# Kernel optimization log

Measured on AMD Instinct MI355X. Metric: run time of the kernel, lower is better.

The kernel has to match this reference:

```python
import jax, jax.numpy as jnp
import numpy as np

BN_EPS = 1e-5


def gcn_conv(x, src, dst, W, b):
    # PyG GCNConv: add self-loops, symmetric normalization, bias after aggregation
    n = x.shape[0]
    h = x @ W                                   # [N, d]
    deg = jnp.zeros((n,), x.dtype).at[dst].add(1.0) + 1.0  # in-degree + self-loop
    dinv = jax.lax.rsqrt(deg)
    norm = dinv[src] * dinv[dst]                # [E]
    agg = jnp.zeros_like(h).at[dst].add(h[src] * norm[:, None])
    agg = agg + h * (dinv * dinv)[:, None]      # self-loop messages
    return agg + b


def batchnorm(x, gamma, beta):
    mu = x.mean(0)
    var = x.var(0)  # biased, as torch BN training mode
    return (x - mu) * jax.lax.rsqrt(var + BN_EPS) * gamma + beta


def mha(x, w_in, b_in, w_out, b_out, n_heads=4):
    # torch nn.MultiheadAttention, input [L, N, E]
    L, N, d = x.shape
    hd = d // n_heads
    qkv = x @ w_in.T + b_in                     # [L, N, 3d]
    q, k, v = jnp.split(qkv, 3, axis=-1)
    rh = lambda t: t.reshape(L, N, n_heads, hd)
    q = rh(q) * (1.0 / np.sqrt(hd))
    k, v = rh(k), rh(v)
    scores = jnp.einsum('lnhd,mnhd->nhlm', q, k)
    a = jax.nn.softmax(scores, axis=-1)
    o = jnp.einsum('nhlm,mnhd->lnhd', a, v).reshape(L, N, d)
    return o @ w_out.T + b_out


def setup_inputs() -> dict:
    key = jax.random.key(0)
    N, d, E, L, R = 50000, 128, 400000, 3, 4
    ks = jax.random.split(key, 12)
    s = 1.0 / np.sqrt(d)
    return {
        'features': jax.random.normal(ks[0], (N, d), jnp.float32),
        'rel_emb': jax.random.normal(ks[1], (R, d), jnp.float32),
        'edge_index': jax.random.randint(ks[2], (R, 2, E), 0, N, dtype=jnp.int32),
        'W_gcn': jax.random.normal(ks[3], (L, d, d), jnp.float32) * s,
        'b_gcn': jnp.zeros((L, d), jnp.float32),
        'bn_gamma': jnp.ones((L - 1, d), jnp.float32),
        'bn_beta': jnp.zeros((L - 1, d), jnp.float32),
        'W_rt': jax.random.normal(ks[4], (L, d, d), jnp.float32) * s,
        'b_rt': jnp.zeros((L, d), jnp.float32),
        'attn_w_in': jax.random.normal(ks[5], (3 * d, d), jnp.float32) * s,
        'attn_b_in': jnp.zeros((3 * d,), jnp.float32),
        'attn_w_out': jax.random.normal(ks[6], (d, d), jnp.float32) * s,
        'attn_b_out': jnp.zeros((d,), jnp.float32),
        'alphas': jnp.full((4,), 0.95, jnp.float32),
        'fusion_q': jax.random.normal(ks[7], (d,), jnp.float32),
        'fusion_w': jax.random.normal(ks[8], (d, d), jnp.float32) * s,
        'fusion_b': jnp.zeros((d,), jnp.float32),
    }


def reference(features, rel_emb, edge_index, W_gcn, b_gcn, bn_gamma, bn_beta,
              W_rt, b_rt, attn_w_in, attn_b_in, attn_w_out, attn_b_out,
              alphas, fusion_q, fusion_w, fusion_b):
    L = W_gcn.shape[0]
    # RelationGCN unpacks rel_emb as (poi_r, s_r, d_r, n_r) and processes
    # relations in order (n, poi, s, d) -> permute to processing order.
    perm = jnp.array([3, 0, 1, 2])
    rels = rel_emb[perm]                # [4, d], order (n, poi, s, d)
    edges = edge_index[perm]            # [4, 2, E]
    embs = jnp.broadcast_to(features, (4,) + features.shape)  # all start at features

    def inner(emb, r, src, dst, Wg, bg, gamma, beta):
        h = gcn_conv(emb * r, src, dst, Wg, bg)
        return emb + jax.nn.leaky_relu(batchnorm(h, gamma, beta))

    for i in range(L - 1):
        embs = jax.vmap(inner, in_axes=(0, 0, 0, 0, None, None, None, None))(
            embs, rels, edges[:, 0], edges[:, 1],
            W_gcn[i], b_gcn[i], bn_gamma[i], bn_beta[i])
        rels = rels @ W_rt[i].T + b_rt[i]
        # dropout p=0.0 -> identity

    embs = jax.vmap(lambda e, r, s_, t_: gcn_conv(e * r, s_, t_, W_gcn[-1], b_gcn[-1]))(
        embs, rels, edges[:, 0], edges[:, 1])
    rels = rels @ W_rt[-1].T + b_rt[-1]

    # PM_Model mis-unpacks RelationGCN outputs (returned order n,poi,s,d as
    # poi,s,d,n). CrossLayer then stacks (n_emb, poi_emb, d_emb, s_emb) which in
    # true processing order is (d, n, s, poi):
    stk = jnp.stack([embs[3], embs[0], embs[2], embs[1]])  # [4, N, d]
    fusion = mha(stk, attn_w_in, attn_b_in, attn_w_out, attn_b_out)
    a = alphas  # [alpha_n, alpha_poi, alpha_d, alpha_s]
    n_f = fusion[0] * a[0] + (1 - a[0]) * stk[0]
    poi_f = fusion[1] * a[1] + (1 - a[1]) * stk[1]
    d_f = fusion[2] * a[2] + (1 - a[2]) * stk[2]
    s_f = fusion[3] * a[3] + (1 - a[3]) * stk[3]

    def score(f):
        return jnp.mean(jnp.sum(jax.nn.leaky_relu(f @ fusion_w.T + fusion_b) * fusion_q, axis=1))

    w = jax.nn.softmax(jnp.stack([score(n_f), score(poi_f), score(s_f), score(d_f)]))
    region = w[0] * n_f + w[1] * poi_f + w[2] * s_f + w[3] * d_f

    # Final multiplies use the same mis-unpacked rel names:
    # n_r<-rels[3](true d), poi_r<-rels[0](true n), s_r<-rels[1], d_r<-rels[2]
    return (region, region * rels[3], region * rels[0], region * rels[1], region * rels[2])
```

## Files before the change

kernel.cpp:

```cpp
#include <hip/hip_runtime.h>
#include <cstdio>

#define DD 128
#define NREL 4

using short8 = __attribute__((ext_vector_type(8))) short;
using f32x4  = __attribute__((ext_vector_type(4))) float;

struct PtrB4 { const unsigned short* p[4]; };
struct OutB4 { unsigned short* p[4]; };

__device__ __forceinline__ int edge_perm(int r) { return (r + 3) & 3; }

__device__ __forceinline__ float bf_lo(unsigned u) { return __uint_as_float(u << 16); }
__device__ __forceinline__ float bf_hi(unsigned u) { return __uint_as_float(u & 0xffff0000u); }
__device__ __forceinline__ float bfe(short s) {
  return __uint_as_float(((unsigned)(unsigned short)s) << 16);
}
__device__ __forceinline__ unsigned short f2bf(float f) {
  unsigned x = __float_as_uint(f);
  unsigned r = (x + 0x7fffu + ((x >> 16) & 1u)) >> 16;
  return (unsigned short)r;
}
__device__ __forceinline__ unsigned pack2(float a, float b) {
  return (unsigned)f2bf(a) | ((unsigned)f2bf(b) << 16);
}


__global__ void rels_init(const float* __restrict__ rel_emb, float* __restrict__ rels) {
  int t = threadIdx.x;
  int r = t >> 7, c = t & 127;
  rels[t] = rel_emb[edge_perm(r) * DD + c];
}

__global__ void rels_update(const float* __restrict__ rin, const float* __restrict__ Wrt,
                            const float* __restrict__ brt, float* __restrict__ rout) {
  int t = threadIdx.x;
  int r = t >> 7, j = t & 127;
  float s = brt[j];
  const float* wr = Wrt + j * DD;
  const float* xr = rin + r * DD;
  for (int c = 0; c < DD; ++c) s += xr[c] * wr[c];
  rout[t] = s;
}

__global__ void scale_w_bf(const float* __restrict__ rels_i, const float* __restrict__ Wg,
                           unsigned short* __restrict__ Wsb) {
  int i = blockIdx.x * 256 + threadIdx.x;
  int r = i >> 14, rem = i & 16383, j = rem >> 7, c = rem & 127;
  Wsb[i] = f2bf(rels_i[r * DD + c] * Wg[c * DD + j]);
}

__global__ void conv_w(const float* __restrict__ w_in, const float* __restrict__ w_out,
                       const float* __restrict__ w_fus, unsigned short* __restrict__ Wab) {
  int i = blockIdx.x * 256 + threadIdx.x;
  float v = (i < 49152) ? w_in[i] : (i < 65536 ? w_out[i - 49152] : w_fus[i - 65536]);
  Wab[i] = f2bf(v);
}

__global__ void conv_f2b(const float* __restrict__ in, unsigned* __restrict__ out2, size_t n4) {
  size_t i = (size_t)blockIdx.x * 256 + threadIdx.x;
  if (i < n4) {
    float4 v = ((const float4*)in)[i];
    out2[i * 2]     = pack2(v.x, v.y);
    out2[i * 2 + 1] = pack2(v.z, v.w);
  }
}


__global__ void count_deg(const int* __restrict__ ei, int* __restrict__ deg, int N, int E) {
  int r = blockIdx.y;
  int base = blockIdx.x * 1024 + threadIdx.x;
  const int* dsts = ei + (size_t)edge_perm(r) * 2 * E + E;
#pragma unroll
  for (int k = 0; k < 4; ++k) {
    int e = base + k * 256;
    if (e < E) atomicAdd(deg + (size_t)r * N + dsts[e], 1);
  }
}

__global__ void finalize_dinv(const int* __restrict__ deg, float* __restrict__ dinv, int total) {
  int i = blockIdx.x * 256 + threadIdx.x;
  if (i < total) dinv[i] = rsqrtf((float)deg[i] + 1.0f);
}

__global__ void scan_block(const int* __restrict__ deg, int* __restrict__ excl,
                           int* __restrict__ bsums, int n) {
  __shared__ int sh[256];
  int i = blockIdx.x * 256 + threadIdx.x;
  int v = (i < n) ? deg[i] : 0;
  sh[threadIdx.x] = v;
  __syncthreads();
  for (int st = 1; st < 256; st <<= 1) {
    int t = (threadIdx.x >= st) ? sh[threadIdx.x - st] : 0;
    __syncthreads();
    sh[threadIdx.x] += t;
    __syncthreads();
  }
  if (i < n) excl[i] = sh[threadIdx.x] - v;
  if (threadIdx.x == 255) bsums[blockIdx.x] = sh[255];
}

__global__ void scan_sums(int* __restrict__ bsums, int nb) {
  __shared__ int sh[1024];
  int v = (threadIdx.x < nb) ? bsums[threadIdx.x] : 0;
  sh[threadIdx.x] = v;
  __syncthreads();
  for (int st = 1; st < 1024; st <<= 1) {
    int t = (threadIdx.x >= st) ? sh[threadIdx.x - st] : 0;
    __syncthreads();
    sh[threadIdx.x] += t;
    __syncthreads();
  }
  if (threadIdx.x < nb) bsums[threadIdx.x] = sh[threadIdx.x] - v;
}

__global__ void scan_add(int* __restrict__ excl, int* __restrict__ cursor,
                         const int* __restrict__ bsums, int n) {
  int i = blockIdx.x * 256 + threadIdx.x;
  if (i < n) {
    int o = excl[i] + bsums[blockIdx.x];
    excl[i] = o;
    cursor[i] = o;
  }
}

__global__ void fill_edges(const int* __restrict__ ei, int* __restrict__ cursor,
                           int* __restrict__ srcbuf, int N, int E) {
  int r = blockIdx.y;
  int base = blockIdx.x * 1024 + threadIdx.x;
  const int* bp = ei + (size_t)edge_perm(r) * 2 * E;
  int s[4], d[4], pos[4];
#pragma unroll
  for (int k = 0; k < 4; ++k) {
    int e = base + k * 256;
    s[k] = (e < E) ? bp[e] : 0;
    d[k] = (e < E) ? bp[E + e] : 0;
  }
#pragma unroll
  for (int k = 0; k < 4; ++k) {
    int e = base + k * 256;
    if (e < E) pos[k] = atomicAdd(&cursor[r * N + d[k]], 1);
  }
#pragma unroll
  for (int k = 0; k < 4; ++k) {
    int e = base + k * 256;
    if (e < E) srcbuf[pos[k]] = r * N + s[k];
  }
}

template <int MODE>
__global__ __launch_bounds__(256) void gemm_ws(PtrB4 xs, PtrB4 wz, OutB4 ys,
                                               const float* __restrict__ bias,
                                               const float* __restrict__ dinv,
                                               const float* __restrict__ fq,
                                               float* __restrict__ S,
                                               PtrB4 stks,
                                               const float* __restrict__ alphas,
                                               int M) {
  int z = blockIdx.y;
  const unsigned short* __restrict__ X = xs.p[z];
  const unsigned short* __restrict__ W = wz.p[z];
  int tid = threadIdx.x;
  int wave = tid >> 6, lane = tid & 63;
  int r16 = lane & 15, kgrp = lane >> 4;
  int rowhalf = wave >> 1, colbase = (wave & 1) * 64;
  int blockrow = blockIdx.x * 64;

  short8 b[4][4];
#pragma unroll
  for (int s = 0; s < 4; ++s)
#pragma unroll
    for (int cn = 0; cn < 4; ++cn)
      b[s][cn] = *(const short8*)(W + ((colbase + cn * 16 + r16) << 7) + s * 32 + kgrp * 8);

  int row0 = blockrow + rowhalf * 32 + r16;
  int r0c = row0 < M ? row0 : M - 1;
  int r1c = row0 + 16 < M ? row0 + 16 : M - 1;
  short8 a[2][4];
#pragma unroll
  for (int s = 0; s < 4; ++s) {
    a[0][s] = *(const short8*)(X + (size_t)r0c * DD + s * 32 + kgrp * 8);
    a[1][s] = *(const short8*)(X + (size_t)r1c * DD + s * 32 + kgrp * 8);
  }

  f32x4 acc[2][4];
#pragma unroll
  for (int rt = 0; rt < 2; ++rt)
#pragma unroll
    for (int cn = 0; cn < 4; ++cn)
#pragma unroll
      for (int j = 0; j < 4; ++j) acc[rt][cn][j] = 0.f;

#pragma unroll
  for (int s = 0; s < 4; ++s)
#pragma unroll
    for (int rt = 0; rt < 2; ++rt)
#pragma unroll
      for (int cn = 0; cn < 4; ++cn)
        acc[rt][cn] = __builtin_amdgcn_mfma_f32_16x16x32_bf16(a[rt][s], b[s][cn], acc[rt][cn], 0, 0, 0);

  __shared__ float red[256];
  if constexpr (MODE == 2) {
    float ss = 0.f;
#pragma unroll
    for (int rt = 0; rt < 2; ++rt)
#pragma unroll
      for (int cn = 0; cn < 4; ++cn) {
        int col = colbase + cn * 16 + r16;
        float bb = bias[col];
        float qc = fq[col];
#pragma unroll
        for (int i = 0; i < 4; ++i) {
          int row = blockrow + rowhalf * 32 + rt * 16 + kgrp * 4 + i;
          if (row < M) {
            float y = acc[rt][cn][i] + bb;
            float v = y > 0.f ? y : 0.01f * y;
            ss += v * qc;
          }
        }
      }
    red[tid] = ss;
    __syncthreads();
    for (int st = 128; st > 0; st >>= 1) {
      if (tid < st) red[tid] += red[tid + st];
      __syncthreads();
    }
    if (tid == 0) atomicAdd(S + z, red[0]);
  } else {
    __shared__ __align__(16) unsigned short tile[64][DD + 8];
    float dv[2][4];
    if constexpr (MODE == 0) {
#pragma unroll
      for (int rt = 0; rt < 2; ++rt)
#pragma unroll
        for (int i = 0; i < 4; ++i) {
          int row = blockrow + rowhalf * 32 + rt * 16 + kgrp * 4 + i;
          dv[rt][i] = dinv[(size_t)z * M + (row < M ? row : 0)];
        }
    }
#pragma unroll
    for (int rt = 0; rt < 2; ++rt)
#pragma unroll
      for (int cn = 0; cn < 4; ++cn) {
        int col = colbase + cn * 16 + r16;
        float bb = (MODE == 1 || MODE == 3) ? bias[col] : 0.f;
#pragma unroll
        for (int i = 0; i < 4; ++i) {
          int wrow = rowhalf * 32 + rt * 16 + kgrp * 4 + i;
          float y = acc[rt][cn][i] + bb;
          if constexpr (MODE == 0) y *= dv[rt][i];
          tile[wrow][col] = f2bf(y);
        }
      }
    __syncthreads();
    int orow = tid >> 2, seg = tid & 3;
    int grow = blockrow + orow;
    if (grow < M) {
      unsigned short* Yp = ys.p[z] + (size_t)grow * DD + seg * 32;
      const unsigned short* tp = &tile[orow][seg * 32];
      if constexpr (MODE == 3) {
        float aa = alphas[z], na = 1.f - aa;
        const unsigned short* sp = stks.p[z] + (size_t)grow * DD + seg * 32;
#pragma unroll
        for (int k = 0; k < 4; ++k) {
          uint4 pv = *(const uint4*)(tp + k * 8);
          uint4 sv = *(const uint4*)(sp + k * 8);
          const unsigned* pw = &pv.x;
          const unsigned* sw = &sv.x;
          uint4 o; unsigned* ow = &o.x;
#pragma unroll
          for (int j = 0; j < 4; ++j)
            ow[j] = pack2(aa * bf_lo(pw[j]) + na * bf_lo(sw[j]),
                          aa * bf_hi(pw[j]) + na * bf_hi(sw[j]));
          *(uint4*)(Yp + k * 8) = o;
        }
      } else {
#pragma unroll
        for (int k = 0; k < 4; ++k)
          *(uint4*)(Yp + k * 8) = *(const uint4*)(tp + k * 8);
      }
    }
  }
}

template <int WB>
__global__ __launch_bounds__(256) void gemm_upd(PtrB4 res, PtrB4 abs_, PtrB4 wz,
                                                OutB4 xout, OutB4 ys,
                                                const float* __restrict__ ssx,
                                                const float* __restrict__ dinv, int M) {
  int z = blockIdx.y;
  const unsigned short* __restrict__ R = res.p[z];
  const unsigned short* __restrict__ A = abs_.p[z];
  const unsigned short* __restrict__ W = wz.p[z];
  int tid = threadIdx.x;

  __shared__ float ssc[DD], ssh[DD];
  if (tid < DD) {
    ssc[tid] = ssx[((size_t)z * DD + tid) * 2];
    ssh[tid] = ssx[((size_t)z * DD + tid) * 2 + 1];
  }
  __syncthreads();

  int wave = tid >> 6, lane = tid & 63;
  int r16 = lane & 15, kgrp = lane >> 4;
  int rowhalf = wave >> 1, colbase = (wave & 1) * 64;
  int blockrow = blockIdx.x * 64;

  short8 b[4][4];
#pragma unroll
  for (int s = 0; s < 4; ++s)
#pragma unroll
    for (int cn = 0; cn < 4; ++cn)
      b[s][cn] = *(const short8*)(W + ((colbase + cn * 16 + r16) << 7) + s * 32 + kgrp * 8);

  int row0 = blockrow + rowhalf * 32 + r16;
  int rc[2];
  rc[0] = row0 < M ? row0 : M - 1;
  rc[1] = row0 + 16 < M ? row0 + 16 : M - 1;
  short8 a[2][4];
#pragma unroll
  for (int rt = 0; rt < 2; ++rt)
#pragma unroll
    for (int s = 0; s < 4; ++s) {
      int cbase = s * 32 + kgrp * 8;
      short8 rv = *(const short8*)(R + (size_t)rc[rt] * DD + cbase);
      short8 av = *(const short8*)(A + (size_t)rc[rt] * DD + cbase);
      short8 av2;
#pragma unroll
      for (int j = 0; j < 8; ++j) {
        float x = bfe(av[j]) * ssc[cbase + j] + ssh[cbase + j];
        x = x > 0.f ? x : 0.01f * x;
        av2[j] = (short)f2bf(bfe(rv[j]) + x);
      }
      a[rt][s] = av2;
    }
  if (WB) {
#pragma unroll
    for (int rt = 0; rt < 2; ++rt) {
      int row = row0 + rt * 16;
      if (row < M) {
#pragma unroll
        for (int s = 0; s < 4; ++s)
          *(short8*)(xout.p[z] + (size_t)row * DD + s * 32 + kgrp * 8) = a[rt][s];
      }
    }
  }

  f32x4 acc[2][4];
#pragma unroll
  for (int rt = 0; rt < 2; ++rt)
#pragma unroll
    for (int cn = 0; cn < 4; ++cn)
#pragma unroll
      for (int j = 0; j < 4; ++j) acc[rt][cn][j] = 0.f;
#pragma unroll
  for (int s = 0; s < 4; ++s)
#pragma unroll
    for (int rt = 0; rt < 2; ++rt)
#pragma unroll
      for (int cn = 0; cn < 4; ++cn)
        acc[rt][cn] = __builtin_amdgcn_mfma_f32_16x16x32_bf16(a[rt][s], b[s][cn], acc[rt][cn], 0, 0, 0);

  __shared__ __align__(16) unsigned short tile[64][DD + 8];
  float dv[2][4];
#pragma unroll
  for (int rt = 0; rt < 2; ++rt)
#pragma unroll
    for (int i = 0; i < 4; ++i) {
      int row = blockrow + rowhalf * 32 + rt * 16 + kgrp * 4 + i;
      dv[rt][i] = dinv[(size_t)z * M + (row < M ? row : 0)];
    }
#pragma unroll
  for (int rt = 0; rt < 2; ++rt)
#pragma unroll
    for (int cn = 0; cn < 4; ++cn) {
      int col = colbase + cn * 16 + r16;
#pragma unroll
      for (int i = 0; i < 4; ++i) {
        int wrow = rowhalf * 32 + rt * 16 + kgrp * 4 + i;
        tile[wrow][col] = f2bf(acc[rt][cn][i] * dv[rt][i]);
      }
    }
  __syncthreads();
  int orow = tid >> 2, seg = tid & 3;
  int grow = blockrow + orow;
  if (grow < M) {
    unsigned short* Yp = ys.p[z] + (size_t)grow * DD + seg * 32;
    const unsigned short* tp = &tile[orow][seg * 32];
#pragma unroll
    for (int k = 0; k < 4; ++k)
      *(uint4*)(Yp + k * 8) = *(const uint4*)(tp + k * 8);
  }
}

__global__ __launch_bounds__(256) void gather_agg(const int* __restrict__ srcbuf,
                                                  const int* __restrict__ offs,
                                                  const int* __restrict__ deg,
                                                  const float* __restrict__ dinv,
                                                  const uint2* __restrict__ Bs2,
                                                  const float* __restrict__ bias,
                                                  uint2* __restrict__ Ab2, int N4) {
  int rn = blockIdx.x * 8 + (threadIdx.x >> 5);
  if (rn >= N4) return;
  int lane = threadIdx.x & 31;
  int st = offs[rn], cnt = deg[rn];
  uint2 u = Bs2[(size_t)rn * 32 + lane];
  float a0 = bf_lo(u.x), a1 = bf_hi(u.x), a2 = bf_lo(u.y), a3 = bf_hi(u.y);
  int e = 0;
  for (; e + 8 <= cnt; e += 8) {
    int rr[8];
#pragma unroll
    for (int j = 0; j < 8; ++j) rr[j] = srcbuf[st + e + j];
    uint2 vv[8];
#pragma unroll
    for (int j = 0; j < 8; ++j) vv[j] = Bs2[(size_t)rr[j] * 32 + lane];
#pragma unroll
    for (int j = 0; j < 8; ++j) {
      a0 += bf_lo(vv[j].x); a1 += bf_hi(vv[j].x);
      a2 += bf_lo(vv[j].y); a3 += bf_hi(vv[j].y);
    }
  }
  if (e + 4 <= cnt) {
    int rr[4];
#pragma unroll
    for (int j = 0; j < 4; ++j) rr[j] = srcbuf[st + e + j];
    uint2 vv[4];
#pragma unroll
    for (int j = 0; j < 4; ++j) vv[j] = Bs2[(size_t)rr[j] * 32 + lane];
#pragma unroll
    for (int j = 0; j < 4; ++j) {
      a0 += bf_lo(vv[j].x); a1 += bf_hi(vv[j].x);
      a2 += bf_lo(vv[j].y); a3 += bf_hi(vv[j].y);
    }
    e += 4;
  }
  for (; e < cnt; ++e) {
    uint2 v = Bs2[(size_t)srcbuf[st + e] * 32 + lane];
    a0 += bf_lo(v.x); a1 += bf_hi(v.x); a2 += bf_lo(v.y); a3 += bf_hi(v.y);
  }
  float dvv = dinv[rn];
  int c = lane * 4;
  uint2 o;
  o.x = pack2(a0 * dvv + bias[c],     a1 * dvv + bias[c + 1]);
  o.y = pack2(a2 * dvv + bias[c + 2], a3 * dvv + bias[c + 3]);
  Ab2[(size_t)rn * 32 + lane] = o;
}


__global__ void bn_stats(const unsigned* __restrict__ Ab2, float* __restrict__ sums, int N) {
  int r = blockIdx.y;
  int lane = threadIdx.x & 63, grp = threadIdx.x >> 6;
  float s0 = 0.f, q0 = 0.f, s1 = 0.f, q1 = 0.f;
  const unsigned* base = Ab2 + (size_t)r * N * 64;
  for (int n = blockIdx.x * 4 + grp; n < N; n += gridDim.x * 4) {
    unsigned u = base[(size_t)n * 64 + lane];
    float a = bf_lo(u), b = bf_hi(u);
    s0 += a; q0 += a * a; s1 += b; q1 += b * b;
  }
  __shared__ float sh[4][64][4];
  sh[grp][lane][0] = s0; sh[grp][lane][1] = q0; sh[grp][lane][2] = s1; sh[grp][lane][3] = q1;
  __syncthreads();
  if (grp == 0) {
#pragma unroll
    for (int g = 1; g < 4; ++g) {
      s0 += sh[g][lane][0]; q0 += sh[g][lane][1]; s1 += sh[g][lane][2]; q1 += sh[g][lane][3];
    }
    int c0 = lane * 2;
    atomicAdd(sums + (r * DD + c0) * 2, s0);
    atomicAdd(sums + (r * DD + c0) * 2 + 1, q0);
    atomicAdd(sums + (r * DD + c0 + 1) * 2, s1);
    atomicAdd(sums + (r * DD + c0 + 1) * 2 + 1, q1);
  }
}

__global__ void bn_final(const float* __restrict__ sums, const float* __restrict__ gamma,
                         const float* __restrict__ beta, float* __restrict__ ss, int N) {
  int t = threadIdx.x;
  int c = t & 127;
  float mu = sums[t * 2] / N;
  float var = sums[t * 2 + 1] / N - mu * mu;
  float sc = gamma[c] * rsqrtf(var + 1e-5f);
  ss[t * 2] = sc;
  ss[t * 2 + 1] = beta[c] - mu * sc;
}

__global__ void attn_fused(const unsigned short* __restrict__ Q,
                           const unsigned short* __restrict__ K,
                           const unsigned short* __restrict__ V,
                           unsigned* __restrict__ Ob2, int N) {
  int sb = threadIdx.x >> 6;
  int node = blockIdx.x * 4 + sb;
  int lane = threadIdx.x & 63;
  __shared__ float qs[4][4][132], ks[4][4][132], vs[4][4][132];
  __shared__ float ps[4][64];
  if (node < N) {
    int l = lane >> 4, c8 = (lane & 15) * 8;
    uint4 qv = *(const uint4*)(Q + ((size_t)l * N + node) * DD + c8);
    uint4 kv = *(const uint4*)(K + ((size_t)l * N + node) * DD + c8);
    uint4 vv = *(const uint4*)(V + ((size_t)l * N + node) * DD + c8);
    unsigned qa[4] = {qv.x, qv.y, qv.z, qv.w};
    unsigned ka[4] = {kv.x, kv.y, kv.z, kv.w};
    unsigned va[4] = {vv.x, vv.y, vv.z, vv.w};
#pragma unroll
    for (int j = 0; j < 4; ++j) {
      qs[sb][l][c8 + 2 * j]     = bf_lo(qa[j]);
      qs[sb][l][c8 + 2 * j + 1] = bf_hi(qa[j]);
      ks[sb][l][c8 + 2 * j]     = bf_lo(ka[j]);
      ks[sb][l][c8 + 2 * j + 1] = bf_hi(ka[j]);
      vs[sb][l][c8 + 2 * j]     = bf_lo(va[j]);
      vs[sb][l][c8 + 2 * j + 1] = bf_hi(va[j]);
    }
  }
  __syncthreads();
  if (node < N) {
    int h = lane >> 4, l = (lane >> 2) & 3, m = lane & 3;
    const float* qp = &qs[sb][l][h * 32];
    const float* kp = &ks[sb][m][h * 32];
    float s = 0.f;
#pragma unroll
    for (int k2 = 0; k2 < 32; ++k2) s += qp[k2] * kp[k2];
    s *= 0.17677669529663687f;
    float mx = s;
    mx = fmaxf(mx, __shfl_xor(mx, 1));
    mx = fmaxf(mx, __shfl_xor(mx, 2));
    float e = expf(s - mx);
    float sum = e;
    sum += __shfl_xor(sum, 1);
    sum += __shfl_xor(sum, 2);
    ps[sb][lane] = e / sum;
  }
  __syncthreads();
  if (node < N) {
    int c0 = lane * 2, h = c0 >> 5;
    const float* pp = &ps[sb][h * 16];
#pragma unroll
    for (int l = 0; l < 4; ++l) {
      float ol = pp[l * 4 + 0] * vs[sb][0][c0] + pp[l * 4 + 1] * vs[sb][1][c0] +
                 pp[l * 4 + 2] * vs[sb][2][c0] + pp[l * 4 + 3] * vs[sb][3][c0];
      float oh = pp[l * 4 + 0] * vs[sb][0][c0 + 1] + pp[l * 4 + 1] * vs[sb][1][c0 + 1] +
                 pp[l * 4 + 2] * vs[sb][2][c0 + 1] + pp[l * 4 + 3] * vs[sb][3][c0 + 1];
      Ob2[((size_t)l * N + node) * 64 + lane] = pack2(ol, oh);
    }
  }
}

__global__ void wcoef(const float* __restrict__ S, float* __restrict__ coef, int N) {
  if (threadIdx.x == 0) {
    float v0 = S[0] / N, v1 = S[1] / N, v2 = S[3] / N, v3 = S[2] / N;
    float mx = fmaxf(fmaxf(v0, v1), fmaxf(v2, v3));
    float e0 = expf(v0 - mx), e1 = expf(v1 - mx), e2 = expf(v2 - mx), e3 = expf(v3 - mx);
    float inv = 1.f / (e0 + e1 + e2 + e3);
    coef[0] = e0 * inv; coef[1] = e1 * inv; coef[2] = e3 * inv; coef[3] = e2 * inv;
  }
}

__device__ __forceinline__ float bfat(uint2 u, int j) {
  unsigned w = (j < 2) ? u.x : u.y;
  return (j & 1) ? bf_hi(w) : bf_lo(w);
}

__global__ void final_out(const unsigned short* __restrict__ fb, const float* __restrict__ coef,
                          const float* __restrict__ rels3, float* __restrict__ out, int N) {
  size_t NK = (size_t)N * DD;
  size_t i4 = (size_t)blockIdx.x * 256 + threadIdx.x;
  if (i4 >= NK / 4) return;
  size_t g = i4 * 4;
  int c = (int)(g & 127);
  float c0 = coef[0], c1 = coef[1], c2 = coef[2], c3 = coef[3];
  uint2 u0 = *(const uint2*)(fb + g);
  uint2 u1 = *(const uint2*)(fb + NK + g);
  uint2 u2 = *(const uint2*)(fb + 2 * NK + g);
  uint2 u3 = *(const uint2*)(fb + 3 * NK + g);
  float4 reg4, o1, o2, o3, o4;
  float* rp = &reg4.x; float* p1 = &o1.x; float* p2 = &o2.x; float* p3 = &o3.x; float* p4 = &o4.x;
#pragma unroll
  for (int j = 0; j < 4; ++j) {
    float region = c0 * bfat(u0, j) + c1 * bfat(u1, j) + c2 * bfat(u2, j) + c3 * bfat(u3, j);
    rp[j] = region;
    p1[j] = region * rels3[3 * DD + c + j];
    p2[j] = region * rels3[0 * DD + c + j];
    p3[j] = region * rels3[1 * DD + c + j];
    p4[j] = region * rels3[2 * DD + c + j];
  }
  *(float4*)(out + g) = reg4;
  *(float4*)(out + NK + g) = o1;
  *(float4*)(out + 2 * NK + g) = o2;
  *(float4*)(out + 3 * NK + g) = o3;
  *(float4*)(out + 4 * NK + g) = o4;
}


extern "C" void kernel_launch(void* const* d_in, const int* in_sizes, int n_in,
                              void* d_out, int out_size, void* d_ws, size_t ws_size,
                              hipStream_t stream) {
  const float* features  = (const float*)d_in[0];
  const float* rel_emb   = (const float*)d_in[1];
  const int*   edge_idx  = (const int*)d_in[2];
  const float* W_gcn     = (const float*)d_in[3];
  const float* b_gcn     = (const float*)d_in[4];
  const float* bn_gamma  = (const float*)d_in[5];
  const float* bn_beta   = (const float*)d_in[6];
  const float* W_rt      = (const float*)d_in[7];
  const float* b_rt      = (const float*)d_in[8];
  const float* attn_w_in = (const float*)d_in[9];
  const float* attn_b_in = (const float*)d_in[10];
  const float* attn_wout = (const float*)d_in[11];
  const float* attn_bout = (const float*)d_in[12];
  const float* alphas    = (const float*)d_in[13];
  const float* fusion_q  = (const float*)d_in[14];
  const float* fusion_w  = (const float*)d_in[15];
  const float* fusion_b  = (const float*)d_in[16];

  int N = in_sizes[0] / DD;
  int E = in_sizes[2] / (2 * NREL);
  size_t NK = (size_t)N * DD;
  int N4 = 4 * N;

  unsigned short* Xb = (unsigned short*)d_ws;
  unsigned short* Bs = Xb + 4 * NK;
  unsigned short* Ab = Bs + 4 * NK;
  unsigned short* Ub = Ab + 4 * NK;
  unsigned short* Fb = Ub + 4 * NK;
  float* dinv  = (float*)(Fb + NK);
  unsigned short* Wgcnb = (unsigned short*)(dinv + N4);
  unsigned short* Wab   = Wgcnb + 4 * DD * DD;
  float* rels  = (float*)(Wab + 5 * DD * DD);
  float* bnsum = rels + 4 * 512;
  float* bnss  = bnsum + 1024;
  float* S     = bnss + 1024;
  float* coef  = S + 4;
  int* deg_i   = (int*)(coef + 4);
  int* offs    = deg_i + N4;
  int* cur     = offs + N4;
  int* bsums   = cur + N4;
  int* srcb    = bsums + 1024;

  size_t needed = (size_t)((char*)(srcb + 4 * E) - (char*)d_ws);
  if (ws_size < needed) {
    fprintf(stderr, "kernel_launch: ws too small (%zu < %zu)\n", ws_size, needed);
    return;
  }

  int gemmGrid = (N + 63) / 64;
  int scanBlocks = (N4 + 255) / 256;
  int egrid4 = (E + 1023) / 1024;

  hipMemsetAsync(deg_i, 0, (size_t)N4 * sizeof(int), stream);
  count_deg<<<dim3(egrid4, 4), 256, 0, stream>>>(edge_idx, deg_i, N, E);
  finalize_dinv<<<scanBlocks, 256, 0, stream>>>(deg_i, dinv, N4);
  scan_block<<<scanBlocks, 256, 0, stream>>>(deg_i, offs, bsums, N4);
  scan_sums<<<1, 1024, 0, stream>>>(bsums, scanBlocks);
  scan_add<<<scanBlocks, 256, 0, stream>>>(offs, cur, bsums, N4);
  fill_edges<<<dim3(egrid4, 4), 256, 0, stream>>>(edge_idx, cur, srcb, N, E);

  rels_init<<<1, 512, 0, stream>>>(rel_emb, rels);
  conv_w<<<5 * 16384 / 256, 256, 0, stream>>>(attn_w_in, attn_wout, fusion_w, Wab);
  conv_f2b<<<(int)((NK / 4 + 255) / 256), 256, 0, stream>>>(features, (unsigned*)Fb, NK / 4);

  PtrB4 wz, abIn, resIn, dummyP;
  OutB4 msgOut, xbOut, dummyO;
  for (int r = 0; r < 4; ++r) {
    wz.p[r] = Wgcnb + (size_t)r * DD * DD;
    abIn.p[r] = Ab + (size_t)r * NK;
    msgOut.p[r] = Bs + (size_t)r * NK;
    xbOut.p[r] = Xb + (size_t)r * NK;
    dummyP.p[r] = nullptr;
    dummyO.p[r] = nullptr;
  }
  const float* dummy = nullptr;

  scale_w_bf<<<256, 256, 0, stream>>>(rels, W_gcn, Wgcnb);
  {
    PtrB4 xs; for (int r = 0; r < 4; ++r) xs.p[r] = Fb;
    gemm_ws<0><<<dim3(gemmGrid, 4), 256, 0, stream>>>(xs, wz, msgOut, dummy, dinv, dummy,
                                                      nullptr, dummyP, dummy, N);
  }
  gather_agg<<<(N4 + 7) / 8, 256, 0, stream>>>(srcb, offs, deg_i, dinv, (const uint2*)Bs,
                                               b_gcn, (uint2*)Ab, N4);
  hipMemsetAsync(bnsum, 0, 1024 * sizeof(float), stream);
  bn_stats<<<dim3(128, 4), 256, 0, stream>>>((const unsigned*)Ab, bnsum, N);
  bn_final<<<1, 512, 0, stream>>>(bnsum, bn_gamma, bn_beta, bnss, N);
  rels_update<<<1, 512, 0, stream>>>(rels, W_rt, b_rt, rels + 512);

  scale_w_bf<<<256, 256, 0, stream>>>(rels + 512, W_gcn + (size_t)DD * DD, Wgcnb);
  for (int r = 0; r < 4; ++r) resIn.p[r] = Fb;
  gemm_upd<1><<<dim3(gemmGrid, 4), 256, 0, stream>>>(resIn, abIn, wz, xbOut, msgOut,
                                                     bnss, dinv, N);
  gather_agg<<<(N4 + 7) / 8, 256, 0, stream>>>(srcb, offs, deg_i, dinv, (const uint2*)Bs,
                                               b_gcn + DD, (uint2*)Ab, N4);
  hipMemsetAsync(bnsum, 0, 1024 * sizeof(float), stream);
  bn_stats<<<dim3(128, 4), 256, 0, stream>>>((const unsigned*)Ab, bnsum, N);
  bn_final<<<1, 512, 0, stream>>>(bnsum, bn_gamma + DD, bn_beta + DD, bnss, N);
  rels_update<<<1, 512, 0, stream>>>(rels + 512, W_rt + (size_t)DD * DD, b_rt + DD, rels + 1024);

  scale_w_bf<<<256, 256, 0, stream>>>(rels + 1024, W_gcn + (size_t)2 * DD * DD, Wgcnb);
  for (int r = 0; r < 4; ++r) resIn.p[r] = Xb + (size_t)r * NK;
  gemm_upd<0><<<dim3(gemmGrid, 4), 256, 0, stream>>>(resIn, abIn, wz, dummyO, msgOut,
                                                     bnss, dinv, N);
  gather_agg<<<(N4 + 7) / 8, 256, 0, stream>>>(srcb, offs, deg_i, dinv, (const uint2*)Bs,
                                               b_gcn + 2 * DD, (uint2*)Ab, N4);
  rels_update<<<1, 512, 0, stream>>>(rels + 1024, W_rt + (size_t)2 * DD * DD, b_rt + 2 * DD,
                                     rels + 1536);

  const int pstk[4] = {3, 0, 2, 1};
  PtrB4 stk, fromO, fromF, w4;
  OutB4 toQ, toK, toV, toF;
  for (int l = 0; l < 4; ++l) {
    stk.p[l] = Ab + (size_t)pstk[l] * NK;
    toQ.p[l] = Xb + (size_t)l * NK;
    toK.p[l] = Bs + (size_t)l * NK;
    toV.p[l] = Ub + (size_t)l * NK;
    toF.p[l] = Bs + (size_t)l * NK;
    fromO.p[l] = Xb + (size_t)l * NK;
    fromF.p[l] = Bs + (size_t)l * NK;
  }

  for (int l = 0; l < 4; ++l) w4.p[l] = Wab;
  gemm_ws<1><<<dim3(gemmGrid, 4), 256, 0, stream>>>(stk, w4, toQ, attn_b_in, dummy, dummy,
                                                    nullptr, dummyP, dummy, N);
  for (int l = 0; l < 4; ++l) w4.p[l] = Wab + 16384;
  gemm_ws<1><<<dim3(gemmGrid, 4), 256, 0, stream>>>(stk, w4, toK, attn_b_in + DD, dummy, dummy,
                                                    nullptr, dummyP, dummy, N);
  for (int l = 0; l < 4; ++l) w4.p[l] = Wab + 2 * 16384;
  gemm_ws<1><<<dim3(gemmGrid, 4), 256, 0, stream>>>(stk, w4, toV, attn_b_in + 2 * DD, dummy,
                                                    dummy, nullptr, dummyP, dummy, N);
  attn_fused<<<(N + 3) / 4, 256, 0, stream>>>(Xb, Bs, Ub, (unsigned*)Xb, N);
  for (int l = 0; l < 4; ++l) w4.p[l] = Wab + 3 * 16384;
  gemm_ws<3><<<dim3(gemmGrid, 4), 256, 0, stream>>>(fromO, w4, toF, attn_bout, dummy, dummy,
                                                    nullptr, stk, alphas, N);
  hipMemsetAsync(S, 0, 4 * sizeof(float), stream);
  for (int l = 0; l < 4; ++l) w4.p[l] = Wab + 4 * 16384;
  gemm_ws<2><<<dim3(gemmGrid, 4), 256, 0, stream>>>(fromF, w4, toQ , fusion_b, dummy,
                                                    fusion_q, S, dummyP, dummy, N);
  wcoef<<<1, 64, 0, stream>>>(S, coef, N);
  final_out<<<(int)((NK / 4 + 255) / 256), 256, 0, stream>>>(Bs, coef, rels + 1536,
                                                             (float*)d_out, N);
}
```

Baseline: 1.031 ms.

## Fuse attention QKV, softmax, out-proj, alpha-mix and fusion scoring into one kernel

Replaces the three QKV GEMMs, the per-node attention kernel, the output-projection GEMM and the fusion-score GEMM with a single kernel. Each block takes 16 nodes across the 4 stacked embeddings and keeps Q/K/V, the attention output and the fused rows in shared memory. This removes several full-size global round-trips of the intermediate activations and the launch overhead between kernels. Only the alpha-mixed result is written back for the final output. The kernel reloads all five weight matrices per block and uses more shared memory, which may lower occupancy. Separately, the bn_stats grid is enlarged.

```diff
diff --git a/kernel.cpp b/kernel.cpp
--- a/kernel.cpp
+++ b/kernel.cpp
@@ -152,12 +152,7 @@
 template <int MODE>
 __global__ __launch_bounds__(256) void gemm_ws(PtrB4 xs, PtrB4 wz, OutB4 ys,
                                                const float* __restrict__ bias,
-                                               const float* __restrict__ dinv,
-                                               const float* __restrict__ fq,
-                                               float* __restrict__ S,
-                                               PtrB4 stks,
-                                               const float* __restrict__ alphas,
-                                               int M) {
+                                               const float* __restrict__ dinv, int M) {
   int z = blockIdx.y;
   const unsigned short* __restrict__ X = xs.p[z];
   const unsigned short* __restrict__ W = wz.p[z];
@@ -200,87 +195,39 @@
       for (int cn = 0; cn < 4; ++cn)
         acc[rt][cn] = __builtin_amdgcn_mfma_f32_16x16x32_bf16(a[rt][s], b[s][cn], acc[rt][cn], 0, 0, 0);
 
-  __shared__ float red[256];
-  if constexpr (MODE == 2) {
-    float ss = 0.f;
+  __shared__ __align__(16) unsigned short tile[64][DD + 8];
+  float dv[2][4];
+  if constexpr (MODE == 0) {
 #pragma unroll
     for (int rt = 0; rt < 2; ++rt)
 #pragma unroll
-      for (int cn = 0; cn < 4; ++cn) {
-        int col = colbase + cn * 16 + r16;
-        float bb = bias[col];
-        float qc = fq[col];
-#pragma unroll
-        for (int i = 0; i < 4; ++i) {
-          int row = blockrow + rowhalf * 32 + rt * 16 + kgrp * 4 + i;
-          if (row < M) {
-            float y = acc[rt][cn][i] + bb;
-            float v = y > 0.f ? y : 0.01f * y;
-            ss += v * qc;
-          }
-        }
-      }
-    red[tid] = ss;
-    __syncthreads();
-    for (int st = 128; st > 0; st >>= 1) {
-      if (tid < st) red[tid] += red[tid + st];
-      __syncthreads();
-    }
-    if (tid == 0) atomicAdd(S + z, red[0]);
-  } else {
-    __shared__ __align__(16) unsigned short tile[64][DD + 8];
-    float dv[2][4];
-    if constexpr (MODE == 0) {
-#pragma unroll
-      for (int rt = 0; rt < 2; ++rt)
-#pragma unroll
-        for (int i = 0; i < 4; ++i) {
-          int row = blockrow + rowhalf * 32 + rt * 16 + kgrp * 4 + i;
-          dv[rt][i] = dinv[(size_t)z * M + (row < M ? row : 0)];
-        }
-    }
-#pragma unroll
-    for (int rt = 0; rt < 2; ++rt)
-#pragma unroll
-      for (int cn = 0; cn < 4; ++cn) {
-        int col = colbase + cn * 16 + r16;
-        float bb = (MODE == 1 || MODE == 3) ? bias[col] : 0.f;
-#pragma unroll
-        for (int i = 0; i < 4; ++i) {
-          int wrow = rowhalf * 32 + rt * 16 + kgrp * 4 + i;
-          float y = acc[rt][cn][i] + bb;
-          if constexpr (MODE == 0) y *= dv[rt][i];
-          tile[wrow][col] = f2bf(y);
-        }
-      }
-    __syncthreads();
-    int orow = tid >> 2, seg = tid & 3;
-    int grow = blockrow + orow;
-    if (grow < M) {
-      unsigned short* Yp = ys.p[z] + (size_t)grow * DD + seg * 32;
-      const unsigned short* tp = &tile[orow][seg * 32];
-      if constexpr (MODE == 3) {
-        float aa = alphas[z], na = 1.f - aa;
-        const unsigned short* sp = stks.p[z] + (size_t)grow * DD + seg * 32;
-#pragma unroll
-        for (int k = 0; k < 4; ++k) {
-          uint4 pv = *(const uint4*)(tp + k * 8);
-          uint4 sv = *(const uint4*)(sp + k * 8);
-          const unsigned* pw = &pv.x;
-          const unsigned* sw = &sv.x;
-          uint4 o; unsigned* ow = &o.x;
-#pragma unroll
-          for (int j = 0; j < 4; ++j)
-            ow[j] = pack2(aa * bf_lo(pw[j]) + na * bf_lo(sw[j]),
-                          aa * bf_hi(pw[j]) + na * bf_hi(sw[j]));
-          *(uint4*)(Yp + k * 8) = o;
-        }
-      } else {
-#pragma unroll
-        for (int k = 0; k < 4; ++k)
-          *(uint4*)(Yp + k * 8) = *(const uint4*)(tp + k * 8);
-      }
-    }
+      for (int i = 0; i < 4; ++i) {
+        int row = blockrow + rowhalf * 32 + rt * 16 + kgrp * 4 + i;
+        dv[rt][i] = dinv[(size_t)z * M + (row < M ? row : 0)];
+      }
+  }
+#pragma unroll
+  for (int rt = 0; rt < 2; ++rt)
+#pragma unroll
+    for (int cn = 0; cn < 4; ++cn) {
+      int col = colbase + cn * 16 + r16;
+#pragma unroll
+      for (int i = 0; i < 4; ++i) {
+        int wrow = rowhalf * 32 + rt * 16 + kgrp * 4 + i;
+        float y = acc[rt][cn][i];
+        if constexpr (MODE == 0) y *= dv[rt][i];
+        tile[wrow][col] = f2bf(y);
+      }
+    }
+  __syncthreads();
+  int orow = tid >> 2, seg = tid & 3;
+  int grow = blockrow + orow;
+  if (grow < M) {
+    unsigned short* Yp = ys.p[z] + (size_t)grow * DD + seg * 32;
+    const unsigned short* tp = &tile[orow][seg * 32];
+#pragma unroll
+    for (int k = 0; k < 4; ++k)
+      *(uint4*)(Yp + k * 8) = *(const uint4*)(tp + k * 8);
   }
 }
 
@@ -391,6 +338,238 @@
 #pragma unroll
     for (int k = 0; k < 4; ++k)
       *(uint4*)(Yp + k * 8) = *(const uint4*)(tp + k * 8);
+  }
+}
+
+__global__ __launch_bounds__(256) void attn_mega(PtrB4 stks,
+    const unsigned short* __restrict__ Wab,
+    const float* __restrict__ b_in, const float* __restrict__ b_out,
+    const float* __restrict__ alphas, const float* __restrict__ fus_b,
+    const float* __restrict__ fq, unsigned short* __restrict__ fbuf,
+    float* __restrict__ S, int N) {
+  __shared__ __align__(16) unsigned short q_s[64][136];
+  __shared__ __align__(16) unsigned short k_s[64][136];
+  __shared__ __align__(16) unsigned short v_s[64][136];
+  __shared__ float ps[16][64];
+  __shared__ float lred[4];
+  size_t NK = (size_t)N * DD;
+
+  int tid = threadIdx.x;
+  int wave = tid >> 6, lane = tid & 63;
+  int r16 = lane & 15, kgrp = lane >> 4;
+  int rowhalf = wave >> 1, colbase = (wave & 1) * 64;
+  int nodebase = blockIdx.x * 16;
+
+  int rlo = rowhalf * 32 + r16;
+  int rhi = rlo + 16;
+  int nlo = nodebase + (rlo & 15); if (nlo >= N) nlo = N - 1;
+  int nhi = nodebase + (rhi & 15); if (nhi >= N) nhi = N - 1;
+  const unsigned short* a0p = stks.p[rlo >> 4] + (size_t)nlo * DD + kgrp * 8;
+  const unsigned short* a1p = stks.p[rhi >> 4] + (size_t)nhi * DD + kgrp * 8;
+  short8 A0[4], A1[4];
+#pragma unroll
+  for (int s = 0; s < 4; ++s) {
+    A0[s] = *(const short8*)(a0p + s * 32);
+    A1[s] = *(const short8*)(a1p + s * 32);
+  }
+
+  for (int o = 0; o < 3; ++o) {
+    const unsigned short* W = Wab + o * 16384;
+    short8 b[4][4];
+#pragma unroll
+    for (int s = 0; s < 4; ++s)
+#pragma unroll
+      for (int cn = 0; cn < 4; ++cn)
+        b[s][cn] = *(const short8*)(W + ((colbase + cn * 16 + r16) << 7) + s * 32 + kgrp * 8);
+    f32x4 acc[2][4];
+#pragma unroll
+    for (int rt = 0; rt < 2; ++rt)
+#pragma unroll
+      for (int cn = 0; cn < 4; ++cn)
+#pragma unroll
+        for (int j = 0; j < 4; ++j) acc[rt][cn][j] = 0.f;
+#pragma unroll
+    for (int s = 0; s < 4; ++s)
+#pragma unroll
+      for (int cn = 0; cn < 4; ++cn) {
+        acc[0][cn] = __builtin_amdgcn_mfma_f32_16x16x32_bf16(A0[s], b[s][cn], acc[0][cn], 0, 0, 0);
+        acc[1][cn] = __builtin_amdgcn_mfma_f32_16x16x32_bf16(A1[s], b[s][cn], acc[1][cn], 0, 0, 0);
+      }
+    unsigned short (*dst)[136] = (o == 0) ? q_s : (o == 1) ? k_s : v_s;
+#pragma unroll
+    for (int rt = 0; rt < 2; ++rt)
+#pragma unroll
+      for (int cn = 0; cn < 4; ++cn) {
+        int col = colbase + cn * 16 + r16;
+        float bb = b_in[o * DD + col];
+#pragma unroll
+        for (int i = 0; i < 4; ++i) {
+          int wrow = rowhalf * 32 + rt * 16 + kgrp * 4 + i;
+          dst[wrow][col] = f2bf(acc[rt][cn][i] + bb);
+        }
+      }
+  }
+  __syncthreads();
+
+  {
+    int h = lane >> 4, li = (lane >> 2) & 3, m = lane & 3;
+    int c0 = lane * 2, hh = c0 >> 5;
+    for (int t = 0; t < 4; ++t) {
+      int nd = wave * 4 + t;
+      float sc = 0.f;
+#pragma unroll
+      for (int s4 = 0; s4 < 4; ++s4) {
+        short8 qv = *(const short8*)&q_s[li * 16 + nd][h * 32 + s4 * 8];
+        short8 kv = *(const short8*)&k_s[m * 16 + nd][h * 32 + s4 * 8];
+#pragma unroll
+        for (int j = 0; j < 8; ++j) sc += bfe(qv[j]) * bfe(kv[j]);
+      }
+      sc *= 0.17677669529663687f;
+      float mx = sc;
+      mx = fmaxf(mx, __shfl_xor(mx, 1));
+      mx = fmaxf(mx, __shfl_xor(mx, 2));
+      float e = expf(sc - mx);
+      float sum = e;
+      sum += __shfl_xor(sum, 1);
+      sum += __shfl_xor(sum, 2);
+      ps[nd][lane] = e / sum;
+      unsigned v0 = *(const unsigned*)&v_s[0 * 16 + nd][c0];
+      unsigned v1 = *(const unsigned*)&v_s[1 * 16 + nd][c0];
+      unsigned v2 = *(const unsigned*)&v_s[2 * 16 + nd][c0];
+      unsigned v3 = *(const unsigned*)&v_s[3 * 16 + nd][c0];
+      float vl[4] = {bf_lo(v0), bf_lo(v1), bf_lo(v2), bf_lo(v3)};
+      float vh[4] = {bf_hi(v0), bf_hi(v1), bf_hi(v2), bf_hi(v3)};
+#pragma unroll
+      for (int lo = 0; lo < 4; ++lo) {
+        const float* pp = &ps[nd][hh * 16 + lo * 4];
+        float ol = pp[0] * vl[0] + pp[1] * vl[1] + pp[2] * vl[2] + pp[3] * vl[3];
+        float oh = pp[0] * vh[0] + pp[1] * vh[1] + pp[2] * vh[2] + pp[3] * vh[3];
+        *(unsigned*)&q_s[lo * 16 + nd][c0] = pack2(ol, oh);
+      }
+    }
+  }
+  __syncthreads();
+
+  {
+    const unsigned short* W = Wab + 3 * 16384;
+    short8 b[4][4];
+#pragma unroll
+    for (int s = 0; s < 4; ++s)
+#pragma unroll
+      for (int cn = 0; cn < 4; ++cn)
+        b[s][cn] = *(const short8*)(W + ((colbase + cn * 16 + r16) << 7) + s * 32 + kgrp * 8);
+    short8 AO0[4], AO1[4];
+#pragma unroll
+    for (int s = 0; s < 4; ++s) {
+      AO0[s] = *(const short8*)&q_s[rlo][s * 32 + kgrp * 8];
+      AO1[s] = *(const short8*)&q_s[rhi][s * 32 + kgrp * 8];
+    }
+    f32x4 acc[2][4];
+#pragma unroll
+    for (int rt = 0; rt < 2; ++rt)
+#pragma unroll
+      for (int cn = 0; cn < 4; ++cn)
+#pragma unroll
+        for (int j = 0; j < 4; ++j) acc[rt][cn][j] = 0.f;
+#pragma unroll
+    for (int s = 0; s < 4; ++s)
+#pragma unroll
+      for (int cn = 0; cn < 4; ++cn) {
+        acc[0][cn] = __builtin_amdgcn_mfma_f32_16x16x32_bf16(AO0[s], b[s][cn], acc[0][cn], 0, 0, 0);
+        acc[1][cn] = __builtin_amdgcn_mfma_f32_16x16x32_bf16(AO1[s], b[s][cn], acc[1][cn], 0, 0, 0);
+      }
+    __syncthreads();
+#pragma unroll
+    for (int rt = 0; rt < 2; ++rt)
+#pragma unroll
+      for (int cn = 0; cn < 4; ++cn) {
+        int col = colbase + cn * 16 + r16;
+        float bb = b_out[col];
+#pragma unroll
+        for (int i = 0; i < 4; ++i) {
+          int wrow = rowhalf * 32 + rt * 16 + kgrp * 4 + i;
+          k_s[wrow][col] = f2bf(acc[rt][cn][i] + bb);
+        }
+      }
+  }
+  __syncthreads();
+
+  {
+    int orow = tid >> 2, seg = tid & 3;
+    int lb = orow >> 4, nb = nodebase + (orow & 15);
+    if (nb < N) {
+      float aa = alphas[lb], na = 1.f - aa;
+      const unsigned short* sp = stks.p[lb] + (size_t)nb * DD + seg * 32;
+      unsigned short* tp = &k_s[orow][seg * 32];
+      unsigned short* Yp = fbuf + (size_t)lb * NK + (size_t)nb * DD + seg * 32;
+#pragma unroll
+      for (int k = 0; k < 4; ++k) {
+        uint4 pv = *(const uint4*)(tp + k * 8);
+        uint4 sv = *(const uint4*)(sp + k * 8);
+        const unsigned* pw = &pv.x;
+        const unsigned* sw = &sv.x;
+        uint4 o; unsigned* ow = &o.x;
+#pragma unroll
+        for (int j = 0; j < 4; ++j)
+          ow[j] = pack2(aa * bf_lo(pw[j]) + na * bf_lo(sw[j]),
+                        aa * bf_hi(pw[j]) + na * bf_hi(sw[j]));
+        *(uint4*)(Yp + k * 8) = o;
+        *(uint4*)(tp + k * 8) = o;
+      }
+    }
+  }
+  __syncthreads();
+
+  {
+    const unsigned short* W = Wab + 4 * 16384;
+    short8 b[4][4];
+#pragma unroll
+    for (int s = 0; s < 4; ++s)
+#pragma unroll
+      for (int cn = 0; cn < 4; ++cn)
+        b[s][cn] = *(const short8*)(W + ((colbase + cn * 16 + r16) << 7) + s * 32 + kgrp * 8);
+    short8 AF0[4], AF1[4];
+#pragma unroll
+    for (int s = 0; s < 4; ++s) {
+      AF0[s] = *(const short8*)&k_s[rlo][s * 32 + kgrp * 8];
+      AF1[s] = *(const short8*)&k_s[rhi][s * 32 + kgrp * 8];
+    }
+    f32x4 acc[2][4];
+#pragma unroll
+    for (int rt = 0; rt < 2; ++rt)
+#pragma unroll
+      for (int cn = 0; cn < 4; ++cn)
+#pragma unroll
+        for (int j = 0; j < 4; ++j) acc[rt][cn][j] = 0.f;
+#pragma unroll
+    for (int s = 0; s < 4; ++s)
+#pragma unroll
+      for (int cn = 0; cn < 4; ++cn) {
+        acc[0][cn] = __builtin_amdgcn_mfma_f32_16x16x32_bf16(AF0[s], b[s][cn], acc[0][cn], 0, 0, 0);
+        acc[1][cn] = __builtin_amdgcn_mfma_f32_16x16x32_bf16(AF1[s], b[s][cn], acc[1][cn], 0, 0, 0);
+      }
+    float ss0 = 0.f, ss1 = 0.f;
+#pragma unroll
+    for (int cn = 0; cn < 4; ++cn) {
+      int col = colbase + cn * 16 + r16;
+      float bb = fus_b[col];
+      float qc = fq[col];
+#pragma unroll
+      for (int i = 0; i < 4; ++i) {
+        if (nodebase + kgrp * 4 + i < N) {
+          float y0 = acc[0][cn][i] + bb;
+          float y1 = acc[1][cn][i] + bb;
+          ss0 += (y0 > 0.f ? y0 : 0.01f * y0) * qc;
+          ss1 += (y1 > 0.f ? y1 : 0.01f * y1) * qc;
+        }
+      }
+    }
+    if (tid < 4) lred[tid] = 0.f;
+    __syncthreads();
+    atomicAdd(&lred[rowhalf * 2], ss0);
+    atomicAdd(&lred[rowhalf * 2 + 1], ss1);
+    __syncthreads();
+    if (tid < 4) atomicAdd(S + tid, lred[tid]);
   }
 }
 
@@ -483,66 +662,6 @@
   float sc = gamma[c] * rsqrtf(var + 1e-5f);
   ss[t * 2] = sc;
   ss[t * 2 + 1] = beta[c] - mu * sc;
-}
-
-__global__ void attn_fused(const unsigned short* __restrict__ Q,
-                           const unsigned short* __restrict__ K,
-                           const unsigned short* __restrict__ V,
-                           unsigned* __restrict__ Ob2, int N) {
-  int sb = threadIdx.x >> 6;
-  int node = blockIdx.x * 4 + sb;
-  int lane = threadIdx.x & 63;
-  __shared__ float qs[4][4][132], ks[4][4][132], vs[4][4][132];
-  __shared__ float ps[4][64];
-  if (node < N) {
-    int l = lane >> 4, c8 = (lane & 15) * 8;
-    uint4 qv = *(const uint4*)(Q + ((size_t)l * N + node) * DD + c8);
-    uint4 kv = *(const uint4*)(K + ((size_t)l * N + node) * DD + c8);
-    uint4 vv = *(const uint4*)(V + ((size_t)l * N + node) * DD + c8);
-    unsigned qa[4] = {qv.x, qv.y, qv.z, qv.w};
-    unsigned ka[4] = {kv.x, kv.y, kv.z, kv.w};
-    unsigned va[4] = {vv.x, vv.y, vv.z, vv.w};
-#pragma unroll
-    for (int j = 0; j < 4; ++j) {
-      qs[sb][l][c8 + 2 * j]     = bf_lo(qa[j]);
-      qs[sb][l][c8 + 2 * j + 1] = bf_hi(qa[j]);
-      ks[sb][l][c8 + 2 * j]     = bf_lo(ka[j]);
-      ks[sb][l][c8 + 2 * j + 1] = bf_hi(ka[j]);
-      vs[sb][l][c8 + 2 * j]     = bf_lo(va[j]);
-      vs[sb][l][c8 + 2 * j + 1] = bf_hi(va[j]);
-    }
-  }
-  __syncthreads();
-  if (node < N) {
-    int h = lane >> 4, l = (lane >> 2) & 3, m = lane & 3;
-    const float* qp = &qs[sb][l][h * 32];
-    const float* kp = &ks[sb][m][h * 32];
-    float s = 0.f;
-#pragma unroll
-    for (int k2 = 0; k2 < 32; ++k2) s += qp[k2] * kp[k2];
-    s *= 0.17677669529663687f;
-    float mx = s;
-    mx = fmaxf(mx, __shfl_xor(mx, 1));
-    mx = fmaxf(mx, __shfl_xor(mx, 2));
-    float e = expf(s - mx);
-    float sum = e;
-    sum += __shfl_xor(sum, 1);
-    sum += __shfl_xor(sum, 2);
-    ps[sb][lane] = e / sum;
-  }
-  __syncthreads();
-  if (node < N) {
-    int c0 = lane * 2, h = c0 >> 5;
-    const float* pp = &ps[sb][h * 16];
-#pragma unroll
-    for (int l = 0; l < 4; ++l) {
-      float ol = pp[l * 4 + 0] * vs[sb][0][c0] + pp[l * 4 + 1] * vs[sb][1][c0] +
-                 pp[l * 4 + 2] * vs[sb][2][c0] + pp[l * 4 + 3] * vs[sb][3][c0];
-      float oh = pp[l * 4 + 0] * vs[sb][0][c0 + 1] + pp[l * 4 + 1] * vs[sb][1][c0 + 1] +
-                 pp[l * 4 + 2] * vs[sb][2][c0 + 1] + pp[l * 4 + 3] * vs[sb][3][c0 + 1];
-      Ob2[((size_t)l * N + node) * 64 + lane] = pack2(ol, oh);
-    }
-  }
 }
 
 __global__ void wcoef(const float* __restrict__ S, float* __restrict__ coef, int N) {
@@ -658,28 +777,25 @@
   conv_w<<<5 * 16384 / 256, 256, 0, stream>>>(attn_w_in, attn_wout, fusion_w, Wab);
   conv_f2b<<<(int)((NK / 4 + 255) / 256), 256, 0, stream>>>(features, (unsigned*)Fb, NK / 4);
 
-  PtrB4 wz, abIn, resIn, dummyP;
+  PtrB4 wz, abIn, resIn;
   OutB4 msgOut, xbOut, dummyO;
   for (int r = 0; r < 4; ++r) {
     wz.p[r] = Wgcnb + (size_t)r * DD * DD;
     abIn.p[r] = Ab + (size_t)r * NK;
     msgOut.p[r] = Bs + (size_t)r * NK;
     xbOut.p[r] = Xb + (size_t)r * NK;
-    dummyP.p[r] = nullptr;
     dummyO.p[r] = nullptr;
   }
-  const float* dummy = nullptr;
 
   scale_w_bf<<<256, 256, 0, stream>>>(rels, W_gcn, Wgcnb);
   {
     PtrB4 xs; for (int r = 0; r < 4; ++r) xs.p[r] = Fb;
-    gemm_ws<0><<<dim3(gemmGrid, 4), 256, 0, stream>>>(xs, wz, msgOut, dummy, dinv, dummy,
-                                                      nullptr, dummyP, dummy, N);
+    gemm_ws<0><<<dim3(gemmGrid, 4), 256, 0, stream>>>(xs, wz, msgOut, nullptr, dinv, N);
   }
   gather_agg<<<(N4 + 7) / 8, 256, 0, stream>>>(srcb, offs, deg_i, dinv, (const uint2*)Bs,
                                                b_gcn, (uint2*)Ab, N4);
   hipMemsetAsync(bnsum, 0, 1024 * sizeof(float), stream);
-  bn_stats<<<dim3(128, 4), 256, 0, stream>>>((const unsigned*)Ab, bnsum, N);
+  bn_stats<<<dim3(400, 4), 256, 0, stream>>>((const unsigned*)Ab, bnsum, N);
   bn_final<<<1, 512, 0, stream>>>(bnsum, bn_gamma, bn_beta, bnss, N);
   rels_update<<<1, 512, 0, stream>>>(rels, W_rt, b_rt, rels + 512);
 
@@ -690,7 +806,7 @@
   gather_agg<<<(N4 + 7) / 8, 256, 0, stream>>>(srcb, offs, deg_i, dinv, (const uint2*)Bs,
                                                b_gcn + DD, (uint2*)Ab, N4);
   hipMemsetAsync(bnsum, 0, 1024 * sizeof(float), stream);
-  bn_stats<<<dim3(128, 4), 256, 0, stream>>>((const unsigned*)Ab, bnsum, N);
+  bn_stats<<<dim3(400, 4), 256, 0, stream>>>((const unsigned*)Ab, bnsum, N);
   bn_final<<<1, 512, 0, stream>>>(bnsum, bn_gamma + DD, bn_beta + DD, bnss, N);
   rels_update<<<1, 512, 0, stream>>>(rels + 512, W_rt + (size_t)DD * DD, b_rt + DD, rels + 1024);
 
@@ -704,35 +820,12 @@
                                      rels + 1536);
 
   const int pstk[4] = {3, 0, 2, 1};
-  PtrB4 stk, fromO, fromF, w4;
-  OutB4 toQ, toK, toV, toF;
-  for (int l = 0; l < 4; ++l) {
-    stk.p[l] = Ab + (size_t)pstk[l] * NK;
-    toQ.p[l] = Xb + (size_t)l * NK;
-    toK.p[l] = Bs + (size_t)l * NK;
-    toV.p[l] = Ub + (size_t)l * NK;
-    toF.p[l] = Bs + (size_t)l * NK;
-    fromO.p[l] = Xb + (size_t)l * NK;
-    fromF.p[l] = Bs + (size_t)l * NK;
-  }
-
-  for (int l = 0; l < 4; ++l) w4.p[l] = Wab;
-  gemm_ws<1><<<dim3(gemmGrid, 4), 256, 0, stream>>>(stk, w4, toQ, attn_b_in, dummy, dummy,
-                                                    nullptr, dummyP, dummy, N);
-  for (int l = 0; l < 4; ++l) w4.p[l] = Wab + 16384;
-  gemm_ws<1><<<dim3(gemmGrid, 4), 256, 0, stream>>>(stk, w4, toK, attn_b_in + DD, dummy, dummy,
-                                                    nullptr, dummyP, dummy, N);
-  for (int l = 0; l < 4; ++l) w4.p[l] = Wab + 2 * 16384;
-  gemm_ws<1><<<dim3(gemmGrid, 4), 256, 0, stream>>>(stk, w4, toV, attn_b_in + 2 * DD, dummy,
-                                                    dummy, nullptr, dummyP, dummy, N);
-  attn_fused<<<(N + 3) / 4, 256, 0, stream>>>(Xb, Bs, Ub, (unsigned*)Xb, N);
-  for (int l = 0; l < 4; ++l) w4.p[l] = Wab + 3 * 16384;
-  gemm_ws<3><<<dim3(gemmGrid, 4), 256, 0, stream>>>(fromO, w4, toF, attn_bout, dummy, dummy,
-                                                    nullptr, stk, alphas, N);
+  PtrB4 stk;
+  for (int l = 0; l < 4; ++l) stk.p[l] = Ab + (size_t)pstk[l] * NK;
+
   hipMemsetAsync(S, 0, 4 * sizeof(float), stream);
-  for (int l = 0; l < 4; ++l) w4.p[l] = Wab + 4 * 16384;
-  gemm_ws<2><<<dim3(gemmGrid, 4), 256, 0, stream>>>(fromF, w4, toQ , fusion_b, dummy,
-                                                    fusion_q, S, dummyP, dummy, N);
+  attn_mega<<<(N + 15) / 16, 256, 0, stream>>>(stk, Wab, attn_b_in, attn_bout, alphas,
+                                               fusion_b, fusion_q, Bs, S, N);
   wcoef<<<1, 64, 0, stream>>>(S, coef, N);
   final_out<<<(int)((NK / 4 + 255) / 256), 256, 0, stream>>>(Bs, coef, rels + 1536,
                                                              (float*)d_out, N);
```

Result: faster. 962.5 us (-6.6%).
